# Kernel optimization log

Hardware: AMD Instinct MI355X
Metric: run time of the kernel (lower is better)

Reference implementation:

```python
import jax, jax.numpy as jnp
import numpy as np

E, U, D, R = 200000, 50000, 128, 32
N2, N1, NU = 100000, 80000, 20000  # hop-2 frontier, hop-1 frontier, unreachable; N1+N2+NU == E
M1, M0 = 1600000, 800000


def setup_inputs() -> dict:
    key = jax.random.key(0)
    ks = jax.random.split(key, 16)
    inp = {
        'ent_emb': jax.random.normal(ks[0], (E, D), jnp.float32) * 0.1,
        'user_emb': jax.random.normal(ks[1], (U, D), jnp.float32) * 0.1,
        'rel_emb': jax.random.normal(ks[2], (R, D), jnp.float32) * 0.1,
        'W_self': jax.random.normal(ks[3], (D, D), jnp.float32) / np.sqrt(D),
        'W_nei': jax.random.normal(ks[4], (D, D), jnp.float32) / np.sqrt(D),
        'b': jnp.zeros((D,), jnp.float32),
        'final_indices': jax.random.randint(ks[5], (N2,), 0, E, jnp.int32),
        'ent_now1': jax.random.randint(ks[6], (N1,), 0, E, jnp.int32),
        'e1_src': jax.random.randint(ks[7], (M1,), 0, N2, jnp.int32),
        'e1_dst': jax.random.randint(ks[8], (M1,), 0, N1, jnp.int32),
        'e1_rel': jax.random.randint(ks[9], (M1,), 0, R, jnp.int32),
        'e0_src': jax.random.randint(ks[10], (M0,), 0, N1, jnp.int32),
        'e0_dst': jax.random.randint(ks[11], (M0,), 0, U, jnp.int32),
        'e0_rel': jax.random.randint(ks[12], (M0,), 0, R, jnp.int32),
        'unreach_idx': jax.random.randint(ks[13], (NU,), 0, E, jnp.int32),
        'order': jax.random.permutation(ks[14], E).astype(jnp.int32),
    }
    return inp


def _rgcn_layer(x, tail, src, dst, rel, W_self, W_nei, b, rel_emb, n_out, activate):
    # self transform: [N, D]
    out = x @ W_self + b
    if tail is not None:
        # gather neighbor reps + relation modulation: [M, D]
        msg = tail[src] * rel_emb[rel]
        agg = jax.ops.segment_sum(msg, dst, num_segments=n_out)
        deg = jax.ops.segment_sum(jnp.ones_like(dst, dtype=x.dtype), dst, num_segments=n_out)
        agg = agg / jnp.clip(deg, 1.0)[:, None]
        out = out + agg @ W_nei
    return jnp.tanh(out) if activate else out


def reference(ent_emb, user_emb, rel_emb, W_self, W_nei, b,
              final_indices, ent_now1, e1_src, e1_dst, e1_rel,
              e0_src, e0_dst, e0_rel, unreach_idx, order):
    # hop 2: raw gathered entity embeddings (deepest frontier)
    h2 = ent_emb[final_indices]                                            # [N2, D]
    # hop 1: RGCN over kg edges from hop-2 frontier
    h1 = _rgcn_layer(ent_emb[ent_now1], h2, e1_src, e1_dst, e1_rel,
                     W_self, W_nei, b, rel_emb, N1, activate=True)          # [N1, D]
    # hop 0: user representations, no activation (activate=False in source)
    user_rep = _rgcn_layer(user_emb, h1, e0_src, e0_dst, e0_rel,
                           W_self, W_nei, b, rel_emb, U, activate=False)    # [U, D]
    # unreachable entities: self-only transform (tail_rep=None)
    unreachable = _rgcn_layer(ent_emb[unreach_idx], None, None, None, None,
                              W_self, W_nei, b, rel_emb, NU, activate=True)  # [NU, D]
    # concat hop reps in forward hop order, then reindex-scatter by entity order
    ent_user_all = jnp.concatenate([h1, h2, unreachable], axis=0)[order]    # [E, D]
    return jnp.concatenate([user_rep, ent_user_all], axis=0)               # [U+E, D]
```

## Files before the change

### kernel.cpp

```cpp
#include <hip/hip_runtime.h>

#define E_  200000
#define U_  50000
#define D_  128
#define R_  32
#define N2_ 100000
#define N1_ 80000
#define NU_ 20000
#define M1_ 1600000
#define M0_ 800000

#define NBUCK1 313
#define NBUCK0 196

__device__ __forceinline__ float4 ld4(const float* p) {
    return *reinterpret_cast<const float4*>(p);
}
__device__ __forceinline__ void st4(float* p, float4 v) {
    *reinterpret_cast<float4*>(p) = v;
}

__device__ __forceinline__ float fast_tanh(float x) {
    float e = __expf(2.0f * x);
    return 1.0f - 2.0f / (e + 1.0f);
}

__global__ __launch_bounds__(256) void gather_rows_k(
    const float* __restrict__ src, const int* __restrict__ idx,
    float* __restrict__ out, int n)
{
    long long gid = (long long)blockIdx.x * blockDim.x + threadIdx.x;
    int i = (int)(gid >> 5);
    int l = (int)(gid & 31);
    if (i >= n) return;
    int s = idx[i];
    st4(out + (long long)i * 128 + l * 4, ld4(src + (long long)s * 128 + l * 4));
}

__global__ __launch_bounds__(256) void hist_k(
    const int* __restrict__ dst, int* __restrict__ cnt, int M)
{
    int i = blockIdx.x * blockDim.x + threadIdx.x;
    if (i < M) atomicAdd(&cnt[dst[i]], 1);
}

__global__ __launch_bounds__(256) void partial_sums_k(
    const int* __restrict__ cnt, int* __restrict__ bsum, int N)
{
    __shared__ int sm[256];
    const int t = threadIdx.x;
    const int base = blockIdx.x * 1024;
    int sum = 0;
    #pragma unroll
    for (int i = 0; i < 4; ++i) {
        int g = base + t + i * 256;
        if (g < N) sum += cnt[g];
    }
    sm[t] = sum;
    __syncthreads();
    #pragma unroll
    for (int s = 128; s > 0; s >>= 1) {
        if (t < s) sm[t] += sm[t + s];
        __syncthreads();
    }
    if (t == 0) bsum[blockIdx.x] = sm[0];
}

__global__ __launch_bounds__(256) void scan_partials_k(
    int* __restrict__ bsum, int NB, int* __restrict__ off, int N)
{
    __shared__ int ls[256];
    const int t = threadIdx.x;
    int v = (t < NB) ? bsum[t] : 0;
    ls[t] = v;
    __syncthreads();
    #pragma unroll
    for (int d = 1; d < 256; d <<= 1) {
        int u = (t >= d) ? ls[t - d] : 0;
        __syncthreads();
        ls[t] += u;
        __syncthreads();
    }
    if (t < NB) bsum[t] = ls[t] - v;
    if (t == 255) off[N] = ls[255];
}

__global__ __launch_bounds__(256) void scan_apply_k(
    const int* __restrict__ cnt, const int* __restrict__ bsum,
    int* __restrict__ off, int* __restrict__ cur, int N)
{
    __shared__ int buf[1024];
    __shared__ int ts[256];
    const int t = threadIdx.x;
    const int base = blockIdx.x * 1024;
    #pragma unroll
    for (int i = 0; i < 4; ++i) {
        int g = base + t + i * 256;
        buf[t + i * 256] = (g < N) ? cnt[g] : 0;
    }
    __syncthreads();
    const int a = buf[t * 4], b = buf[t * 4 + 1], c = buf[t * 4 + 2], d = buf[t * 4 + 3];
    const int s = a + b + c + d;
    ts[t] = s;
    __syncthreads();
    #pragma unroll
    for (int dd = 1; dd < 256; dd <<= 1) {
        int u = (t >= dd) ? ts[t - dd] : 0;
        __syncthreads();
        ts[t] += u;
        __syncthreads();
    }
    const int pre = bsum[blockIdx.x] + ts[t] - s;
    const int o0 = pre, o1 = pre + a, o2 = o1 + b, o3 = o2 + c;
    const int g0 = base + t * 4;
    if (g0 + 3 < N) {
        *reinterpret_cast<int4*>(off + g0) = make_int4(o0, o1, o2, o3);
        *reinterpret_cast<int4*>(cur + g0) = make_int4(o0, o1, o2, o3);
    } else {
        if (g0     < N) { off[g0]     = o0; cur[g0]     = o0; }
        if (g0 + 1 < N) { off[g0 + 1] = o1; cur[g0 + 1] = o1; }
        if (g0 + 2 < N) { off[g0 + 2] = o2; cur[g0 + 2] = o2; }
    }
}

__global__ __launch_bounds__(256) void init_bcur_k(
    const int* __restrict__ off, int* __restrict__ bcur, int nbuck)
{
    int i = blockIdx.x * blockDim.x + threadIdx.x;
    if (i < nbuck) bcur[i] = off[i << 8];
}

#define EPB 2048
__global__ __launch_bounds__(256) void bin_k(
    const int* __restrict__ src, const int* __restrict__ dst,
    const int* __restrict__ rel, int* __restrict__ bcur,
    int* __restrict__ bdst, int* __restrict__ bsr, int M, int nbuck)
{
    __shared__ int hist[384];
    __shared__ int base[384];
    const int t = threadIdx.x;
    const int e0 = blockIdx.x * EPB;
    for (int i = t; i < nbuck; i += 256) hist[i] = 0;
    __syncthreads();
    int dv[8], sv[8], rv[8];
    #pragma unroll
    for (int i = 0; i < 8; ++i) {
        int e = e0 + i * 256 + t;
        if (e < M) {
            dv[i] = dst[e]; sv[i] = src[e]; rv[i] = rel[e];
            atomicAdd(&hist[dv[i] >> 8], 1);
        } else dv[i] = -1;
    }
    __syncthreads();
    for (int i = t; i < nbuck; i += 256) {
        int c = hist[i];
        base[i] = c ? atomicAdd(&bcur[i], c) : 0;
        hist[i] = 0;
    }
    __syncthreads();
    #pragma unroll
    for (int i = 0; i < 8; ++i) {
        if (dv[i] >= 0) {
            int bk = dv[i] >> 8;
            int p = base[bk] + atomicAdd(&hist[bk], 1);
            bdst[p] = dv[i];
            bsr[p] = sv[i] | (rv[i] << 20);
        }
    }
}

__global__ __launch_bounds__(256) void fill2_k(
    const int* __restrict__ bdst, const int* __restrict__ bsr,
    const int* __restrict__ off, int* __restrict__ cur,
    int* __restrict__ sorted, int N)
{
    int b = blockIdx.x;
    int rs = off[b << 8];
    int reidx = (b + 1) << 8;
    if (reidx > N) reidx = N;
    int re = off[reidx];
    for (int j = rs + threadIdx.x; j < re; j += 256) {
        int d = bdst[j];
        int p = atomicAdd(&cur[d], 1);
        sorted[p] = bsr[j];
    }
}

__global__ __launch_bounds__(256) void seg_reduce_k(
    const float* __restrict__ tail, const float* __restrict__ rel_emb,
    const int* __restrict__ off, const int* __restrict__ sorted,
    float* __restrict__ aggout, int N)
{
    long long gid = (long long)blockIdx.x * blockDim.x + threadIdx.x;
    int row = (int)(gid >> 5);
    int l = (int)(gid & 31) * 4;
    if (row >= N) return;
    int s = off[row], e = off[row + 1];
    float4 acc = make_float4(0.f, 0.f, 0.f, 0.f);
    int j = s;
    for (; j + 1 < e; j += 2) {
        int p0 = sorted[j], p1 = sorted[j + 1];
        float4 t0 = ld4(tail + (long long)(p0 & 0xFFFFF) * 128 + l);
        float4 r0 = ld4(rel_emb + (long long)(p0 >> 20) * 128 + l);
        float4 t1 = ld4(tail + (long long)(p1 & 0xFFFFF) * 128 + l);
        float4 r1 = ld4(rel_emb + (long long)(p1 >> 20) * 128 + l);
        acc.x = fmaf(t0.x, r0.x, acc.x); acc.y = fmaf(t0.y, r0.y, acc.y);
        acc.z = fmaf(t0.z, r0.z, acc.z); acc.w = fmaf(t0.w, r0.w, acc.w);
        acc.x = fmaf(t1.x, r1.x, acc.x); acc.y = fmaf(t1.y, r1.y, acc.y);
        acc.z = fmaf(t1.z, r1.z, acc.z); acc.w = fmaf(t1.w, r1.w, acc.w);
    }
    if (j < e) {
        int p0 = sorted[j];
        float4 t0 = ld4(tail + (long long)(p0 & 0xFFFFF) * 128 + l);
        float4 r0 = ld4(rel_emb + (long long)(p0 >> 20) * 128 + l);
        acc.x = fmaf(t0.x, r0.x, acc.x); acc.y = fmaf(t0.y, r0.y, acc.y);
        acc.z = fmaf(t0.z, r0.z, acc.z); acc.w = fmaf(t0.w, r0.w, acc.w);
    }
    float sc = 1.0f / (float)max(e - s, 1);
    acc.x *= sc; acc.y *= sc; acc.z *= sc; acc.w *= sc;
    st4(aggout + (long long)row * 128 + l, acc);
}

template<bool GATHER, bool BIAS, bool ACT>
__global__ __launch_bounds__(256, 4) void gemm_rows_k(
    const float* __restrict__ X, const int* __restrict__ idx,
    const float* __restrict__ W, const float* __restrict__ bias,
    float* __restrict__ Out, int N)
{
    __shared__ float XsT[32][128];
    __shared__ float Ws [32][128];
    const int tid = threadIdx.x;
    const int rowbase = blockIdx.x * 128;
    const int r0 = (tid >> 4) * 8;
    const int c4 = (tid & 15) * 4;

    float acc[8][8];
    #pragma unroll
    for (int j = 0; j < 8; ++j) {
        float bv = BIAS ? bias[(j < 4) ? (c4 + j) : (c4 + 64 + j - 4)] : 0.0f;
        #pragma unroll
        for (int i = 0; i < 8; ++i) acc[i][j] = bv;
    }

    const int srow = tid >> 3;
    const int skq  = (tid & 7) * 4;
    const int sswz = (tid & 7) << 2;
    const int wkk  = tid >> 5;
    const int wcc  = (tid & 31) * 4;

    int cl[4], gi[4];
    #pragma unroll
    for (int p = 0; p < 4; ++p) {
        int grow = rowbase + p * 32 + srow;
        cl[p] = grow < N ? grow : (N - 1);
        gi[p] = GATHER ? idx[cl[p]] : cl[p];
    }

    for (int k0 = 0; k0 < 128; k0 += 32) {
        __syncthreads();
        #pragma unroll
        for (int p = 0; p < 4; ++p) {
            float4 v = ld4(X + (long long)gi[p] * 128 + k0 + skq);
            int rs = (p * 32 + srow) ^ sswz;
            XsT[skq + 0][rs] = v.x;
            XsT[skq + 1][rs] = v.y;
            XsT[skq + 2][rs] = v.z;
            XsT[skq + 3][rs] = v.w;
        }
        #pragma unroll
        for (int p = 0; p < 4; ++p) {
            int k = p * 8 + wkk;
            st4(&Ws[k][wcc], ld4(W + (long long)(k0 + k) * 128 + wcc));
        }
        __syncthreads();
        #pragma unroll
        for (int k = 0; k < 32; ++k) {
            int A0 = (((r0 >> 2) ^ ((k >> 2) & 7)) << 2);
            float4 x0 = ld4(&XsT[k][A0]);
            float4 x1 = ld4(&XsT[k][A0 ^ 4]);
            float4 w0 = ld4(&Ws[k][c4]);
            float4 w1 = ld4(&Ws[k][c4 + 64]);
            float xs[8] = {x0.x, x0.y, x0.z, x0.w, x1.x, x1.y, x1.z, x1.w};
            float ws[8] = {w0.x, w0.y, w0.z, w0.w, w1.x, w1.y, w1.z, w1.w};
            #pragma unroll
            for (int i = 0; i < 8; ++i)
                #pragma unroll
                for (int j = 0; j < 8; ++j)
                    acc[i][j] = fmaf(xs[i], ws[j], acc[i][j]);
        }
    }

    #pragma unroll
    for (int i = 0; i < 8; ++i) {
        int row = rowbase + r0 + i;
        if (row >= N) continue;
        float* op = Out + (long long)row * 128;
        float vals[8];
        #pragma unroll
        for (int j = 0; j < 8; ++j) vals[j] = acc[i][j];
        if (ACT) {
            #pragma unroll
            for (int j = 0; j < 8; ++j) vals[j] = fast_tanh(vals[j]);
        }
        st4(op + c4,      make_float4(vals[0], vals[1], vals[2], vals[3]));
        st4(op + c4 + 64, make_float4(vals[4], vals[5], vals[6], vals[7]));
    }
}

template<bool GATHER1, bool ACT>
__global__ __launch_bounds__(256, 4) void gemm_cat_k(
    const float* __restrict__ X1, const int* __restrict__ idx,
    const float* __restrict__ X2,
    const float* __restrict__ W1, const float* __restrict__ W2,
    const float* __restrict__ bias, float* __restrict__ Out, int N)
{
    __shared__ float XsT[32][128];
    __shared__ float Ws [32][128];
    const int tid = threadIdx.x;
    const int rowbase = blockIdx.x * 128;
    const int r0 = (tid >> 4) * 8;
    const int c4 = (tid & 15) * 4;

    float acc[8][8];
    #pragma unroll
    for (int j = 0; j < 8; ++j) {
        float bv = bias[(j < 4) ? (c4 + j) : (c4 + 64 + j - 4)];
        #pragma unroll
        for (int i = 0; i < 8; ++i) acc[i][j] = bv;
    }

    const int srow = tid >> 3;
    const int skq  = (tid & 7) * 4;
    const int sswz = (tid & 7) << 2;
    const int wkk  = tid >> 5;
    const int wcc  = (tid & 31) * 4;

    int cl[4], gi[4];
    #pragma unroll
    for (int p = 0; p < 4; ++p) {
        int grow = rowbase + p * 32 + srow;
        cl[p] = grow < N ? grow : (N - 1);
        gi[p] = GATHER1 ? idx[cl[p]] : cl[p];
    }

    for (int cc = 0; cc < 8; ++cc) {
        __syncthreads();
        #pragma unroll
        for (int p = 0; p < 4; ++p) {
            const float* xr;
            if (cc < 4) xr = X1 + (long long)gi[p] * 128 + cc * 32;
            else        xr = X2 + (long long)cl[p] * 128 + (cc - 4) * 32;
            float4 v = ld4(xr + skq);
            int rs = (p * 32 + srow) ^ sswz;
            XsT[skq + 0][rs] = v.x;
            XsT[skq + 1][rs] = v.y;
            XsT[skq + 2][rs] = v.z;
            XsT[skq + 3][rs] = v.w;
        }
        #pragma unroll
        for (int p = 0; p < 4; ++p) {
            int k = p * 8 + wkk;
            const float* wsrc = (cc < 4)
                ? (W1 + (long long)(cc * 32 + k) * 128)
                : (W2 + (long long)((cc - 4) * 32 + k) * 128);
            st4(&Ws[k][wcc], ld4(wsrc + wcc));
        }
        __syncthreads();
        #pragma unroll
        for (int k = 0; k < 32; ++k) {
            int A0 = (((r0 >> 2) ^ ((k >> 2) & 7)) << 2);
            float4 x0 = ld4(&XsT[k][A0]);
            float4 x1 = ld4(&XsT[k][A0 ^ 4]);
            float4 w0 = ld4(&Ws[k][c4]);
            float4 w1 = ld4(&Ws[k][c4 + 64]);
            float xs[8] = {x0.x, x0.y, x0.z, x0.w, x1.x, x1.y, x1.z, x1.w};
            float ws[8] = {w0.x, w0.y, w0.z, w0.w, w1.x, w1.y, w1.z, w1.w};
            #pragma unroll
            for (int i = 0; i < 8; ++i)
                #pragma unroll
                for (int j = 0; j < 8; ++j)
                    acc[i][j] = fmaf(xs[i], ws[j], acc[i][j]);
        }
    }

    #pragma unroll
    for (int i = 0; i < 8; ++i) {
        int row = rowbase + r0 + i;
        if (row >= N) continue;
        float* op = Out + (long long)row * 128;
        float vals[8];
        #pragma unroll
        for (int j = 0; j < 8; ++j) vals[j] = acc[i][j];
        if (ACT) {
            #pragma unroll
            for (int j = 0; j < 8; ++j) vals[j] = fast_tanh(vals[j]);
        }
        st4(op + c4,      make_float4(vals[0], vals[1], vals[2], vals[3]));
        st4(op + c4 + 64, make_float4(vals[4], vals[5], vals[6], vals[7]));
    }
}

extern "C" void kernel_launch(void* const* d_in, const int* in_sizes, int n_in,
                              void* d_out, int out_size, void* d_ws, size_t ws_size,
                              hipStream_t stream)
{
    const float* ent_emb  = (const float*)d_in[0];
    const float* user_emb = (const float*)d_in[1];
    const float* rel_emb  = (const float*)d_in[2];
    const float* W_self   = (const float*)d_in[3];
    const float* W_nei    = (const float*)d_in[4];
    const float* bvec     = (const float*)d_in[5];
    const int* final_indices = (const int*)d_in[6];
    const int* ent_now1   = (const int*)d_in[7];
    const int* e1_src     = (const int*)d_in[8];
    const int* e1_dst     = (const int*)d_in[9];
    const int* e1_rel     = (const int*)d_in[10];
    const int* e0_src     = (const int*)d_in[11];
    const int* e0_dst     = (const int*)d_in[12];
    const int* e0_rel     = (const int*)d_in[13];
    const int* unreach_idx = (const int*)d_in[14];
    const int* order      = (const int*)d_in[15];

    float* out = (float*)d_out;
    float* ws  = (float*)d_ws;

    float* concat = ws;
    float* agg1 = concat + (size_t)E_ * 128;
    float* agg0 = agg1 + (size_t)N1_ * 128;
    int* cur1 = (int*)(agg0 + (size_t)U_ * 128);
    int* cur0 = cur1 + N1_;
    int* off1 = cur0 + U_;
    int* off0 = off1 + (N1_ + 4);
    int* bsum1 = off0 + (U_ + 4);
    int* bsum0 = bsum1 + 256;
    int* bcur1 = bsum0 + 256;
    int* bcur0 = bcur1 + 320;
    int* sorted1 = bcur0 + 320;
    int* sorted0 = sorted1 + M1_;

    int* bdst = (int*)agg1;
    int* bsr  = bdst + M1_;

    float* h1   = concat;
    float* h2   = concat + (size_t)N1_ * 128;
    float* unre = concat + (size_t)(N1_ + N2_) * 128;

    const int NB1 = (N1_ + 1023) / 1024;
    const int NB0 = (U_  + 1023) / 1024;

    hipMemsetAsync(cur1, 0, (size_t)(N1_ + U_) * sizeof(int), stream);

    gather_rows_k<<<(N2_ * 32 + 255) / 256, 256, 0, stream>>>(
        ent_emb, final_indices, h2, N2_);

    hist_k<<<(M1_ + 255) / 256, 256, 0, stream>>>(e1_dst, cur1, M1_);
    partial_sums_k<<<NB1, 256, 0, stream>>>(cur1, bsum1, N1_);
    scan_partials_k<<<1, 256, 0, stream>>>(bsum1, NB1, off1, N1_);
    scan_apply_k<<<NB1, 256, 0, stream>>>(cur1, bsum1, off1, cur1, N1_);
    init_bcur_k<<<2, 256, 0, stream>>>(off1, bcur1, NBUCK1);
    bin_k<<<(M1_ + EPB - 1) / EPB, 256, 0, stream>>>(
        e1_src, e1_dst, e1_rel, bcur1, bdst, bsr, M1_, NBUCK1);
    fill2_k<<<NBUCK1, 256, 0, stream>>>(bdst, bsr, off1, cur1, sorted1, N1_);
    seg_reduce_k<<<(N1_ * 32 + 255) / 256, 256, 0, stream>>>(
        h2, rel_emb, off1, sorted1, agg1, N1_);

    gemm_cat_k<true, true><<<(N1_ + 127) / 128, 256, 0, stream>>>(
        ent_emb, ent_now1, agg1, W_self, W_nei, bvec, h1, N1_);

    hist_k<<<(M0_ + 255) / 256, 256, 0, stream>>>(e0_dst, cur0, M0_);
    partial_sums_k<<<NB0, 256, 0, stream>>>(cur0, bsum0, U_);
    scan_partials_k<<<1, 256, 0, stream>>>(bsum0, NB0, off0, U_);
    scan_apply_k<<<NB0, 256, 0, stream>>>(cur0, bsum0, off0, cur0, U_);
    init_bcur_k<<<1, 256, 0, stream>>>(off0, bcur0, NBUCK0);
    bin_k<<<(M0_ + EPB - 1) / EPB, 256, 0, stream>>>(
        e0_src, e0_dst, e0_rel, bcur0, bdst, bsr, M0_, NBUCK0);
    fill2_k<<<NBUCK0, 256, 0, stream>>>(bdst, bsr, off0, cur0, sorted0, U_);
    seg_reduce_k<<<(U_ * 32 + 255) / 256, 256, 0, stream>>>(
        h1, rel_emb, off0, sorted0, agg0, U_);

    gemm_cat_k<false, false><<<(U_ + 127) / 128, 256, 0, stream>>>(
        user_emb, nullptr, agg0, W_self, W_nei, bvec, out, U_);

    gemm_rows_k<true, true, true><<<(NU_ + 127) / 128, 256, 0, stream>>>(
        ent_emb, unreach_idx, W_self, bvec, unre, NU_);

    gather_rows_k<<<(E_ * 32 + 255) / 256, 256, 0, stream>>>(
        concat, order, out + (size_t)U_ * 128, E_);
}
```

Baseline: 988.7 us.

## Double-buffer shared-memory tiles in concatenated GEMM to overlap loads with FMA

The two-weight GEMM kernel now uses two shared-memory buffers for the X and W tiles. Global loads for the next K chunk are issued into registers before the FMA loop on the current chunk, then stored to the other buffer, so only one barrier is needed per chunk instead of two. The swizzle index is rewritten in an equivalent, simpler form in both GEMM kernels. The cost is double the LDS footprint and extra live registers, with the launch-bounds occupancy hint lowered from 4 to 2 blocks.

After: 1.987 ms. 101% more time.

```diff
diff --git a/kernel.cpp b/kernel.cpp
--- a/kernel.cpp
+++ b/kernel.cpp
@@ -275,7 +275,7 @@
         __syncthreads();
         #pragma unroll
         for (int k = 0; k < 32; ++k) {
-            int A0 = (((r0 >> 2) ^ ((k >> 2) & 7)) << 2);
+            int A0 = r0 ^ (k & 28);
             float4 x0 = ld4(&XsT[k][A0]);
             float4 x1 = ld4(&XsT[k][A0 ^ 4]);
             float4 w0 = ld4(&Ws[k][c4]);
@@ -308,14 +308,14 @@
 }
 
 template<bool GATHER1, bool ACT>
-__global__ __launch_bounds__(256, 4) void gemm_cat_k(
+__global__ __launch_bounds__(256, 2) void gemm_cat_k(
     const float* __restrict__ X1, const int* __restrict__ idx,
     const float* __restrict__ X2,
     const float* __restrict__ W1, const float* __restrict__ W2,
     const float* __restrict__ bias, float* __restrict__ Out, int N)
 {
-    __shared__ float XsT[32][128];
-    __shared__ float Ws [32][128];
+    __shared__ float XsT[2][32][128];
+    __shared__ float Ws [2][32][128];
     const int tid = threadIdx.x;
     const int rowbase = blockIdx.x * 128;
     const int r0 = (tid >> 4) * 8;
@@ -331,7 +331,6 @@
 
     const int srow = tid >> 3;
     const int skq  = (tid & 7) * 4;
-    const int sswz = (tid & 7) << 2;
     const int wkk  = tid >> 5;
     const int wcc  = (tid & 31) * 4;
 
@@ -343,36 +342,51 @@
         gi[p] = GATHER1 ? idx[cl[p]] : cl[p];
     }
 
+    auto ldx = [&](int cc, int p) -> float4 {
+        int k0 = (cc & 3) * 32;
+        const float* base = (cc < 4) ? X1 + (long long)gi[p] * 128
+                                     : X2 + (long long)cl[p] * 128;
+        return ld4(base + k0 + skq);
+    };
+    auto ldw = [&](int cc, int p) -> float4 {
+        int k0 = (cc & 3) * 32;
+        const float* base = (cc < 4) ? W1 : W2;
+        return ld4(base + (long long)(k0 + p * 8 + wkk) * 128 + wcc);
+    };
+    auto store_chunk = [&](int buf, const float4* xv, const float4* wv) {
+        #pragma unroll
+        for (int p = 0; p < 4; ++p) {
+            int rs = (p * 32 + srow) ^ skq;
+            XsT[buf][skq + 0][rs] = xv[p].x;
+            XsT[buf][skq + 1][rs] = xv[p].y;
+            XsT[buf][skq + 2][rs] = xv[p].z;
+            XsT[buf][skq + 3][rs] = xv[p].w;
+            st4(&Ws[buf][p * 8 + wkk][wcc], wv[p]);
+        }
+    };
+
+    {
+        float4 xv[4], wv[4];
+        #pragma unroll
+        for (int p = 0; p < 4; ++p) { xv[p] = ldx(0, p); wv[p] = ldw(0, p); }
+        store_chunk(0, xv, wv);
+    }
+    __syncthreads();
+
+    int cur = 0;
     for (int cc = 0; cc < 8; ++cc) {
-        __syncthreads();
-        #pragma unroll
-        for (int p = 0; p < 4; ++p) {
-            const float* xr;
-            if (cc < 4) xr = X1 + (long long)gi[p] * 128 + cc * 32;
-            else        xr = X2 + (long long)cl[p] * 128 + (cc - 4) * 32;
-            float4 v = ld4(xr + skq);
-            int rs = (p * 32 + srow) ^ sswz;
-            XsT[skq + 0][rs] = v.x;
-            XsT[skq + 1][rs] = v.y;
-            XsT[skq + 2][rs] = v.z;
-            XsT[skq + 3][rs] = v.w;
-        }
-        #pragma unroll
-        for (int p = 0; p < 4; ++p) {
-            int k = p * 8 + wkk;
-            const float* wsrc = (cc < 4)
-                ? (W1 + (long long)(cc * 32 + k) * 128)
-                : (W2 + (long long)((cc - 4) * 32 + k) * 128);
-            st4(&Ws[k][wcc], ld4(wsrc + wcc));
-        }
-        __syncthreads();
+        float4 xv[4], wv[4];
+        if (cc < 7) {
+            #pragma unroll
+            for (int p = 0; p < 4; ++p) { xv[p] = ldx(cc + 1, p); wv[p] = ldw(cc + 1, p); }
+        }
         #pragma unroll
         for (int k = 0; k < 32; ++k) {
-            int A0 = (((r0 >> 2) ^ ((k >> 2) & 7)) << 2);
-            float4 x0 = ld4(&XsT[k][A0]);
-            float4 x1 = ld4(&XsT[k][A0 ^ 4]);
-            float4 w0 = ld4(&Ws[k][c4]);
-            float4 w1 = ld4(&Ws[k][c4 + 64]);
+            int A0 = r0 ^ (k & 28);
+            float4 x0 = ld4(&XsT[cur][k][A0]);
+            float4 x1 = ld4(&XsT[cur][k][A0 ^ 4]);
+            float4 w0 = ld4(&Ws[cur][k][c4]);
+            float4 w1 = ld4(&Ws[cur][k][c4 + 64]);
             float xs[8] = {x0.x, x0.y, x0.z, x0.w, x1.x, x1.y, x1.z, x1.w};
             float ws[8] = {w0.x, w0.y, w0.z, w0.w, w1.x, w1.y, w1.z, w1.w};
             #pragma unroll
@@ -380,6 +394,11 @@
                 #pragma unroll
                 for (int j = 0; j < 8; ++j)
                     acc[i][j] = fmaf(xs[i], ws[j], acc[i][j]);
+        }
+        if (cc < 7) {
+            store_chunk(cur ^ 1, xv, wv);
+            __syncthreads();
+            cur ^= 1;
         }
     }
 
```
